# Kernel optimization log

Hardware: AMD Instinct MI355X
Metric: run time of the kernel (lower is better)

The kernel has to match this reference:

```python
import jax, jax.numpy as jnp
import numpy as np

N = 8192   # nodes
F = 128    # features
ORDER = 4  # polynomial taps


def setup_inputs() -> dict:
    key = jax.random.key(0)
    k1, k2, k3 = jax.random.split(key, 3)
    X = jax.random.normal(k1, (N, F), dtype=jnp.float32)
    # scale GSO so powers don't blow up (spectral-norm-ish normalization)
    S = jax.random.normal(k2, (N, N), dtype=jnp.float32) / jnp.sqrt(jnp.float32(N))
    coefficients = jax.random.uniform(k3, (ORDER,), dtype=jnp.float32)
    return {"X": X, "S": S, "coefficients": coefficients}


def reference(X, S, coefficients):
    # y = sum_{k=0}^{K-1} h_k * S^k X
    Z = X
    y = coefficients[0] * Z
    for k in range(1, ORDER):  # small fixed tap count; loop over taps, not data
        Z = S @ Z              # S^k X, [N, F]
        y = y + coefficients[k] * Z
    return y
```

## Files before the change

kernel.cpp:

```cpp
#include <hip/hip_runtime.h>
#include <hip/hip_bf16.h>
#include <stdint.h>


typedef __attribute__((ext_vector_type(8))) short     bf16x8;
typedef __attribute__((ext_vector_type(8))) uint16_t  u16x8;
typedef __attribute__((ext_vector_type(4))) float     f32x4;

#define NN 8192
#define NF 128
#define ZSTRIDE (8192 + 64)

#define WAITV(n) asm volatile("s_waitcnt vmcnt(" #n ")" ::: "memory")
#define WAITL0   asm volatile("s_waitcnt lgkmcnt(0)" ::: "memory")

__device__ inline uint16_t f2bf(float f) {
    uint32_t u = __builtin_bit_cast(uint32_t, f);
    u += 0x7fffu + ((u >> 16) & 1u);
    return (uint16_t)(u >> 16);
}

__device__ inline void gl2lds16(const void* g, uint8_t* l) {
    __builtin_amdgcn_global_load_lds(
        (const __attribute__((address_space(1))) uint32_t*)g,
        (__attribute__((address_space(3))) uint32_t*)l,
        16, 0, 0);
}

__device__ inline bf16x8 ld16(const uint8_t* p) {
    return __builtin_bit_cast(bf16x8, *(const u16x8*)p);
}

__global__ __launch_bounds__(256) void k_prep(const float* __restrict__ X,
                                              const float* __restrict__ coeff,
                                              float* __restrict__ y,
                                              uint16_t* __restrict__ ZT0) {
    __shared__ float tile[16][NF + 4];
    const int t  = threadIdx.x;
    const int r0 = blockIdx.x * 16;
    const float h0 = coeff[0];
#pragma unroll
    for (int i = 0; i < 2; ++i) {
        int o   = (i * 256 + t) * 4;
        int row = o >> 7, col = o & 127;
        f32x4 v = *(const f32x4*)(X + (size_t)(r0 + row) * NF + col);
        *(f32x4*)&tile[row][col] = v;
        *(f32x4*)(y + (size_t)(r0 + row) * NF + col) = v * h0;
    }
    __syncthreads();
    const int c = t >> 1, rh = t & 1;
    u16x8 pk;
#pragma unroll
    for (int e = 0; e < 8; ++e) pk[e] = f2bf(tile[rh * 8 + e][c]);
    *(u16x8*)(ZT0 + (size_t)c * ZSTRIDE + r0 + rh * 8) = pk;
}

template<int NT>
__device__ inline void gemm_core(const uint16_t* asrc, const uint16_t* bsrc,
                                 uint8_t* smem, int t, f32x4 (&acc)[4],
                                 int aoff, int bof) {
    auto stage = [&](int buf, int kt) {
        const int ko = kt * 64;
        uint8_t* b = smem + buf * 24576;
        gl2lds16(asrc + ko, b + t * 16);
        gl2lds16(bsrc + ko, b + 8192 + t * 16);
        gl2lds16(bsrc + (size_t)64 * ZSTRIDE + ko, b + 16384 + t * 16);
    };
    stage(0, 0);
    int cur = 0;
#pragma unroll 1
    for (int kt = 0; kt < NT; ++kt) {
        if (kt + 1 < NT) {
            stage(cur ^ 1, kt + 1);
            WAITV(3);
        } else {
            WAITV(0);
        }
        __builtin_amdgcn_s_barrier();
        __builtin_amdgcn_sched_barrier(0);
        const uint8_t* bb = smem + cur * 24576;
        bf16x8 a0 = ld16(bb + aoff);
        bf16x8 a1 = ld16(bb + (aoff ^ 64));
#pragma unroll
        for (int ct = 0; ct < 4; ++ct) {
            acc[ct] = __builtin_amdgcn_mfma_f32_16x16x32_bf16(
                a0, ld16(bb + bof + ct * 16 * 128), acc[ct], 0, 0, 0);
            acc[ct] = __builtin_amdgcn_mfma_f32_16x16x32_bf16(
                a1, ld16(bb + ((bof + ct * 16 * 128) ^ 64)), acc[ct], 0, 0, 0);
        }
        WAITL0;
        __builtin_amdgcn_sched_barrier(0);
        __builtin_amdgcn_s_barrier();
        cur ^= 1;
    }
}

template<int KS>
__global__ __launch_bounds__(512, 4) void k_gemm_bf(
    const uint16_t* __restrict__ S16, const uint16_t* __restrict__ ZTin,
    float* __restrict__ P)
{
    __shared__ __align__(16) uint8_t smem[2][24576];
    const int t = threadIdx.x, lane = t & 63;
    const int w = t >> 6, m = lane & 15, g = lane >> 4;
    const int rt = w & 3, ch = w >> 2;
    const int mt = blockIdx.x & 127, ks = blockIdx.x >> 7;
    const int r0 = mt * 64;
    const int kb = ks * (NN / KS);
    constexpr int NT = (NN / KS) / 64;

    const int srow = t >> 3, sc = t & 7;
    const int scs  = (sc ^ (srow & 7)) << 3;
    const uint16_t* asrc = S16  + (size_t)(r0 + srow) * NN + kb + scs;
    const uint16_t* bsrc = ZTin + (size_t)srow * ZSTRIDE   + kb + scs;

    const int sw   = m & 7;
    const int aoff = (rt * 16 + m) * 128 + ((g ^ sw) << 4);
    const int bof  = 8192 + (ch * 64 + m) * 128 + ((g ^ sw) << 4);

    f32x4 acc[4] = {};
    gemm_core<NT>(asrc, bsrc, &smem[0][0], t, acc, aoff, bof);

    float* pb = P + ((size_t)ks * NN + r0 + rt * 16 + 4 * g) * NF + ch * 64 + m;
#pragma unroll
    for (int ct = 0; ct < 4; ++ct)
#pragma unroll
        for (int i = 0; i < 4; ++i)
            pb[(size_t)i * NF + ct * 16] = acc[ct][i];
}

template<int KS>
__global__ __launch_bounds__(512, 4) void k_gemm_cv2(
    const float* __restrict__ Sf, const uint16_t* __restrict__ S16,
    const uint16_t* __restrict__ ZTin, float* __restrict__ P)
{
    __shared__ __align__(16) uint8_t smem[2][24576];
    const int t = threadIdx.x, lane = t & 63;
    const int w = t >> 6, m = lane & 15, g = lane >> 4;
    const int rt = w & 3, ch = w >> 2;
    const int mt = blockIdx.x & 127, ks = blockIdx.x >> 7;
    const int r0 = mt * 64;
    const int kb = ks * (NN / KS);
    constexpr int KSL = NN / KS;
    constexpr int NT  = KSL / 64;
    constexpr int C8  = KSL / 8;
    constexpr int ITERS = 64 * KSL / (512 * 8);

    uint16_t* S16w = (uint16_t*)S16;
#pragma unroll 4
    for (int it = 0; it < ITERS; ++it) {
        int id  = it * 512 + t;
        int row = id / C8, c8 = id % C8;
        size_t off = (size_t)(r0 + row) * NN + kb + c8 * 8;
        f32x4 a = *(const f32x4*)(Sf + off);
        f32x4 b = *(const f32x4*)(Sf + off + 4);
        u16x8 p;
#pragma unroll
        for (int j = 0; j < 4; ++j) { p[j] = f2bf(a[j]); p[j + 4] = f2bf(b[j]); }
        *(u16x8*)(S16w + off) = p;
    }
    WAITV(0);
    __syncthreads();

    const int srow = t >> 3, sc = t & 7;
    const int scs  = (sc ^ (srow & 7)) << 3;
    const uint16_t* asrc = S16  + (size_t)(r0 + srow) * NN + kb + scs;
    const uint16_t* bsrc = ZTin + (size_t)srow * ZSTRIDE   + kb + scs;

    const int sw   = m & 7;
    const int aoff = (rt * 16 + m) * 128 + ((g ^ sw) << 4);
    const int bof  = 8192 + (ch * 64 + m) * 128 + ((g ^ sw) << 4);

    f32x4 acc[4] = {};
    gemm_core<NT>(asrc, bsrc, &smem[0][0], t, acc, aoff, bof);

    float* pb = P + ((size_t)ks * NN + r0 + rt * 16 + 4 * g) * NF + ch * 64 + m;
#pragma unroll
    for (int ct = 0; ct < 4; ++ct)
#pragma unroll
        for (int i = 0; i < 4; ++i)
            pb[(size_t)i * NF + ct * 16] = acc[ct][i];
}

template<int KS, bool WRITE_ZT>
__global__ __launch_bounds__(256) void k_combine(const float* __restrict__ P,
                                                 float* __restrict__ y,
                                                 uint16_t* __restrict__ ZTout,
                                                 const float* __restrict__ coeff,
                                                 int pass) {
    __shared__ float tile[16][NF + 4];
    const int t = threadIdx.x, r0 = blockIdx.x * 16;
    const float hk = coeff[pass];
    const int row = t >> 4, col = (t & 15) * 8;
    const size_t off = (size_t)(r0 + row) * NF + col;
    f32x4 s0 = *(const f32x4*)(P + off);
    f32x4 s1 = *(const f32x4*)(P + off + 4);
#pragma unroll
    for (int k = 1; k < KS; ++k) {
        s0 += *(const f32x4*)(P + (size_t)k * NN * NF + off);
        s1 += *(const f32x4*)(P + (size_t)k * NN * NF + off + 4);
    }
    float* yp = y + off;
    f32x4 y0 = *(const f32x4*)yp, y1 = *(const f32x4*)(yp + 4);
    *(f32x4*)yp       = y0 + hk * s0;
    *(f32x4*)(yp + 4) = y1 + hk * s1;
    if (WRITE_ZT) {
        *(f32x4*)&tile[row][col]     = s0;
        *(f32x4*)&tile[row][col + 4] = s1;
        __syncthreads();
        const int c = t >> 1, rh = t & 1;
        u16x8 pk;
#pragma unroll
        for (int e = 0; e < 8; ++e) pk[e] = f2bf(tile[rh * 8 + e][c]);
        *(u16x8*)(ZTout + (size_t)c * ZSTRIDE + r0 + rh * 8) = pk;
    }
}

template<int KS>
static void run(const float* X, const float* S, const float* coeff, float* y,
                uint16_t* ZT0, uint16_t* ZT1, uint16_t* S16, float* P,
                hipStream_t stream) {
    k_prep<<<dim3(512), dim3(256), 0, stream>>>(X, coeff, y, ZT0);
    k_gemm_cv2<KS><<<dim3(128 * KS), dim3(512), 0, stream>>>(S, S16, ZT0, P);
    k_combine<KS, true ><<<dim3(512), dim3(256), 0, stream>>>(P, y, ZT1, coeff, 1);
    k_gemm_bf<KS><<<dim3(128 * KS), dim3(512), 0, stream>>>(S16, ZT1, P);
    k_combine<KS, true ><<<dim3(512), dim3(256), 0, stream>>>(P, y, ZT0, coeff, 2);
    k_gemm_bf<KS><<<dim3(128 * KS), dim3(512), 0, stream>>>(S16, ZT0, P);
    k_combine<KS, false><<<dim3(512), dim3(256), 0, stream>>>(P, y, nullptr, coeff, 3);
}

extern "C" void kernel_launch(void* const* d_in, const int* in_sizes, int n_in,
                              void* d_out, int out_size, void* d_ws, size_t ws_size,
                              hipStream_t stream) {
    const float* X     = (const float*)d_in[0];
    const float* S     = (const float*)d_in[1];
    const float* coeff = (const float*)d_in[2];
    float* y = (float*)d_out;

    uint8_t* ws = (uint8_t*)d_ws;
    const size_t zb     = ((size_t)NF * ZSTRIDE * sizeof(uint16_t) + 255) & ~(size_t)255;
    const size_t s16b   = (size_t)NN * NN * sizeof(uint16_t);
    const size_t base   = 2 * zb + s16b;
    const size_t pslice = (size_t)NN * NF * sizeof(float);
    uint16_t* ZT0 = (uint16_t*)ws;
    uint16_t* ZT1 = (uint16_t*)(ws + zb);
    uint16_t* S16 = (uint16_t*)(ws + 2 * zb);
    float*    P   = (float*)(ws + base);

    if (ws_size >= base + 4 * pslice)
        run<4>(X, S, coeff, y, ZT0, ZT1, S16, P, stream);
    else if (ws_size >= base + 2 * pslice)
        run<2>(X, S, coeff, y, ZT0, ZT1, S16, P, stream);
    else
        run<1>(X, S, coeff, y, ZT0, ZT1, S16, P, stream);
}
```

Before: 196.1 us.

## Fuse all stages into one persistent kernel with atomic grid barriers

Replaces the seven-launch sequence (prep, three GEMMs, three combines) with a single persistent kernel of 512 blocks that moves between stages using atomic-counter grid barriers. The barrier counters are zeroed with a memset before each launch. The goal is to remove per-launch overhead and the tail and idle time between dependent kernels. The risk is deadlock if all 512 blocks cannot be co-resident, plus spin-wait cost at each barrier. The fallback path now converts S to bf16 in a separate kernel instead of inside the first GEMM.

Result: slower. 673.9 us (+243.7%).

```diff
diff --git a/kernel.cpp b/kernel.cpp
--- a/kernel.cpp
+++ b/kernel.cpp
@@ -10,6 +10,7 @@
 #define NN 8192
 #define NF 128
 #define ZSTRIDE (8192 + 64)
+#define GRID 512
 
 #define WAITV(n) asm volatile("s_waitcnt vmcnt(" #n ")" ::: "memory")
 #define WAITL0   asm volatile("s_waitcnt lgkmcnt(0)" ::: "memory")
@@ -31,28 +32,20 @@
     return __builtin_bit_cast(bf16x8, *(const u16x8*)p);
 }
 
-__global__ __launch_bounds__(256) void k_prep(const float* __restrict__ X,
-                                              const float* __restrict__ coeff,
-                                              float* __restrict__ y,
-                                              uint16_t* __restrict__ ZT0) {
-    __shared__ float tile[16][NF + 4];
-    const int t  = threadIdx.x;
-    const int r0 = blockIdx.x * 16;
-    const float h0 = coeff[0];
-#pragma unroll
-    for (int i = 0; i < 2; ++i) {
-        int o   = (i * 256 + t) * 4;
-        int row = o >> 7, col = o & 127;
-        f32x4 v = *(const f32x4*)(X + (size_t)(r0 + row) * NF + col);
-        *(f32x4*)&tile[row][col] = v;
-        *(f32x4*)(y + (size_t)(r0 + row) * NF + col) = v * h0;
-    }
+__device__ inline void gridbar(uint32_t* ctr, int idx) {
     __syncthreads();
-    const int c = t >> 1, rh = t & 1;
-    u16x8 pk;
-#pragma unroll
-    for (int e = 0; e < 8; ++e) pk[e] = f2bf(tile[rh * 8 + e][c]);
-    *(u16x8*)(ZT0 + (size_t)c * ZSTRIDE + r0 + rh * 8) = pk;
+    if (threadIdx.x == 0) {
+        __threadfence();
+        __hip_atomic_fetch_add(ctr + idx, 1u, __ATOMIC_ACQ_REL,
+                               __HIP_MEMORY_SCOPE_AGENT);
+        uint32_t v;
+        do {
+            __builtin_amdgcn_s_sleep(2);
+            v = __hip_atomic_load(ctr + idx, __ATOMIC_ACQUIRE,
+                                  __HIP_MEMORY_SCOPE_AGENT);
+        } while (v < GRID);
+    }
+    __syncthreads();
 }
 
 template<int NT>
@@ -95,6 +88,149 @@
     }
 }
 
+
+__device__ void mega_gemm(const uint16_t* S16, const uint16_t* ZTin,
+                          float* P, uint8_t* smem, int mt, int ks, int t) {
+    const int lane = t & 63, w = t >> 6, m = lane & 15, g = lane >> 4;
+    const int rt = w & 3, ch = w >> 2;
+    const int r0 = mt * 64, kb = ks * 2048;
+    const int srow = t >> 3, sc = t & 7;
+    const int scs  = (sc ^ (srow & 7)) << 3;
+    const uint16_t* asrc = S16  + (size_t)(r0 + srow) * NN + kb + scs;
+    const uint16_t* bsrc = ZTin + (size_t)srow * ZSTRIDE   + kb + scs;
+    const int sw   = m & 7;
+    const int aoff = (rt * 16 + m) * 128 + ((g ^ sw) << 4);
+    const int bof  = 8192 + (ch * 64 + m) * 128 + ((g ^ sw) << 4);
+    f32x4 acc[4] = {};
+    gemm_core<32>(asrc, bsrc, smem, t, acc, aoff, bof);
+    float* pb = P + ((size_t)ks * NN + r0 + rt * 16 + 4 * g) * NF + ch * 64 + m;
+#pragma unroll
+    for (int ct = 0; ct < 4; ++ct)
+#pragma unroll
+        for (int i = 0; i < 4; ++i)
+            pb[(size_t)i * NF + ct * 16] = acc[ct][i];
+}
+
+__device__ void mega_combine(const float* P, float* y, uint16_t* ZTout,
+                             float hk, uint8_t* smem, int bx, int t) {
+    float* tile = (float*)smem;
+    const int r0 = bx * 16;
+    const int row = t >> 5, colc = t & 31;
+    const size_t off = (size_t)(r0 + row) * NF + colc * 4;
+    f32x4 s = *(const f32x4*)(P + off);
+#pragma unroll
+    for (int k = 1; k < 4; ++k)
+        s += *(const f32x4*)(P + (size_t)k * NN * NF + off);
+    f32x4 yv = *(const f32x4*)(y + off);
+    *(f32x4*)(y + off) = yv + hk * s;
+    if (ZTout) {
+        *(f32x4*)&tile[row * 132 + colc * 4] = s;
+        __syncthreads();
+        if (t < 256) {
+            const int c = t >> 1, rh = t & 1;
+            u16x8 pk;
+#pragma unroll
+            for (int e = 0; e < 8; ++e) pk[e] = f2bf(tile[(rh * 8 + e) * 132 + c]);
+            *(u16x8*)(ZTout + (size_t)c * ZSTRIDE + r0 + rh * 8) = pk;
+        }
+    }
+}
+
+__global__ __launch_bounds__(512, 4) void k_mega(
+    const float* __restrict__ S, const float* __restrict__ X,
+    const float* __restrict__ coeff, float* __restrict__ y,
+    uint16_t* ZT0, uint16_t* ZT1, uint16_t* S16, float* P, uint32_t* bar)
+{
+    __shared__ __align__(16) uint8_t smem[49152];
+    const int bx = blockIdx.x, t = threadIdx.x;
+    const int mt = bx & 127, ks = bx >> 7;
+    const int r0 = mt * 64, kb = ks * 2048;
+
+#pragma unroll 4
+    for (int it = 0; it < 32; ++it) {
+        int id  = it * 512 + t;
+        int row = id >> 8, c8 = id & 255;
+        size_t off = (size_t)(r0 + row) * NN + kb + c8 * 8;
+        f32x4 a = *(const f32x4*)(S + off);
+        f32x4 b = *(const f32x4*)(S + off + 4);
+        u16x8 p;
+#pragma unroll
+        for (int j = 0; j < 4; ++j) { p[j] = f2bf(a[j]); p[j + 4] = f2bf(b[j]); }
+        *(u16x8*)(S16 + off) = p;
+    }
+    {
+        float* tile = (float*)smem;
+        const int rp = bx * 16;
+        const float h0 = coeff[0];
+        const int row = t >> 5, colc = t & 31;
+        f32x4 v = *(const f32x4*)(X + (size_t)(rp + row) * NF + colc * 4);
+        *(f32x4*)&tile[row * 132 + colc * 4] = v;
+        *(f32x4*)(y + (size_t)(rp + row) * NF + colc * 4) = v * h0;
+        __syncthreads();
+        if (t < 256) {
+            const int c = t >> 1, rh = t & 1;
+            u16x8 pk;
+#pragma unroll
+            for (int e = 0; e < 8; ++e) pk[e] = f2bf(tile[(rh * 8 + e) * 132 + c]);
+            *(u16x8*)(ZT0 + (size_t)c * ZSTRIDE + rp + rh * 8) = pk;
+        }
+    }
+    gridbar(bar, 0);
+
+    mega_gemm(S16, ZT0, P, smem, mt, ks, t);
+    gridbar(bar, 1);
+    mega_combine(P, y, ZT1, coeff[1], smem, bx, t);
+    gridbar(bar, 2);
+
+    mega_gemm(S16, ZT1, P, smem, mt, ks, t);
+    gridbar(bar, 3);
+    mega_combine(P, y, ZT0, coeff[2], smem, bx, t);
+    gridbar(bar, 4);
+
+    mega_gemm(S16, ZT0, P, smem, mt, ks, t);
+    gridbar(bar, 5);
+    mega_combine(P, y, nullptr, coeff[3], smem, bx, t);
+}
+
+
+__global__ __launch_bounds__(256) void k_convert(const float* __restrict__ S,
+                                                 uint16_t* __restrict__ S16) {
+    const size_t n8 = (size_t)NN * NN / 8;
+    const size_t stride = (size_t)gridDim.x * 256;
+    for (size_t i = (size_t)blockIdx.x * 256 + threadIdx.x; i < n8; i += stride) {
+        f32x4 a = *(const f32x4*)(S + i * 8);
+        f32x4 b = *(const f32x4*)(S + i * 8 + 4);
+        u16x8 p;
+#pragma unroll
+        for (int j = 0; j < 4; ++j) { p[j] = f2bf(a[j]); p[j + 4] = f2bf(b[j]); }
+        *(u16x8*)(S16 + i * 8) = p;
+    }
+}
+
+__global__ __launch_bounds__(256) void k_prep(const float* __restrict__ X,
+                                              const float* __restrict__ coeff,
+                                              float* __restrict__ y,
+                                              uint16_t* __restrict__ ZT0) {
+    __shared__ float tile[16][NF + 4];
+    const int t  = threadIdx.x;
+    const int r0 = blockIdx.x * 16;
+    const float h0 = coeff[0];
+#pragma unroll
+    for (int i = 0; i < 2; ++i) {
+        int o   = (i * 256 + t) * 4;
+        int row = o >> 7, col = o & 127;
+        f32x4 v = *(const f32x4*)(X + (size_t)(r0 + row) * NF + col);
+        *(f32x4*)&tile[row][col] = v;
+        *(f32x4*)(y + (size_t)(r0 + row) * NF + col) = v * h0;
+    }
+    __syncthreads();
+    const int c = t >> 1, rh = t & 1;
+    u16x8 pk;
+#pragma unroll
+    for (int e = 0; e < 8; ++e) pk[e] = f2bf(tile[rh * 8 + e][c]);
+    *(u16x8*)(ZT0 + (size_t)c * ZSTRIDE + r0 + rh * 8) = pk;
+}
+
 template<int KS>
 __global__ __launch_bounds__(512, 4) void k_gemm_bf(
     const uint16_t* __restrict__ S16, const uint16_t* __restrict__ ZTin,
@@ -129,59 +265,6 @@
             pb[(size_t)i * NF + ct * 16] = acc[ct][i];
 }
 
-template<int KS>
-__global__ __launch_bounds__(512, 4) void k_gemm_cv2(
-    const float* __restrict__ Sf, const uint16_t* __restrict__ S16,
-    const uint16_t* __restrict__ ZTin, float* __restrict__ P)
-{
-    __shared__ __align__(16) uint8_t smem[2][24576];
-    const int t = threadIdx.x, lane = t & 63;
-    const int w = t >> 6, m = lane & 15, g = lane >> 4;
-    const int rt = w & 3, ch = w >> 2;
-    const int mt = blockIdx.x & 127, ks = blockIdx.x >> 7;
-    const int r0 = mt * 64;
-    const int kb = ks * (NN / KS);
-    constexpr int KSL = NN / KS;
-    constexpr int NT  = KSL / 64;
-    constexpr int C8  = KSL / 8;
-    constexpr int ITERS = 64 * KSL / (512 * 8);
-
-    uint16_t* S16w = (uint16_t*)S16;
-#pragma unroll 4
-    for (int it = 0; it < ITERS; ++it) {
-        int id  = it * 512 + t;
-        int row = id / C8, c8 = id % C8;
-        size_t off = (size_t)(r0 + row) * NN + kb + c8 * 8;
-        f32x4 a = *(const f32x4*)(Sf + off);
-        f32x4 b = *(const f32x4*)(Sf + off + 4);
-        u16x8 p;
-#pragma unroll
-        for (int j = 0; j < 4; ++j) { p[j] = f2bf(a[j]); p[j + 4] = f2bf(b[j]); }
-        *(u16x8*)(S16w + off) = p;
-    }
-    WAITV(0);
-    __syncthreads();
-
-    const int srow = t >> 3, sc = t & 7;
-    const int scs  = (sc ^ (srow & 7)) << 3;
-    const uint16_t* asrc = S16  + (size_t)(r0 + srow) * NN + kb + scs;
-    const uint16_t* bsrc = ZTin + (size_t)srow * ZSTRIDE   + kb + scs;
-
-    const int sw   = m & 7;
-    const int aoff = (rt * 16 + m) * 128 + ((g ^ sw) << 4);
-    const int bof  = 8192 + (ch * 64 + m) * 128 + ((g ^ sw) << 4);
-
-    f32x4 acc[4] = {};
-    gemm_core<NT>(asrc, bsrc, &smem[0][0], t, acc, aoff, bof);
-
-    float* pb = P + ((size_t)ks * NN + r0 + rt * 16 + 4 * g) * NF + ch * 64 + m;
-#pragma unroll
-    for (int ct = 0; ct < 4; ++ct)
-#pragma unroll
-        for (int i = 0; i < 4; ++i)
-            pb[(size_t)i * NF + ct * 16] = acc[ct][i];
-}
-
 template<int KS, bool WRITE_ZT>
 __global__ __launch_bounds__(256) void k_combine(const float* __restrict__ P,
                                                  float* __restrict__ y,
@@ -217,11 +300,12 @@
 }
 
 template<int KS>
-static void run(const float* X, const float* S, const float* coeff, float* y,
-                uint16_t* ZT0, uint16_t* ZT1, uint16_t* S16, float* P,
-                hipStream_t stream) {
+static void run_fallback(const float* X, const float* S, const float* coeff,
+                         float* y, uint16_t* ZT0, uint16_t* ZT1, uint16_t* S16,
+                         float* P, hipStream_t stream) {
     k_prep<<<dim3(512), dim3(256), 0, stream>>>(X, coeff, y, ZT0);
-    k_gemm_cv2<KS><<<dim3(128 * KS), dim3(512), 0, stream>>>(S, S16, ZT0, P);
+    k_convert<<<dim3(2048), dim3(256), 0, stream>>>(S, S16);
+    k_gemm_bf<KS><<<dim3(128 * KS), dim3(512), 0, stream>>>(S16, ZT0, P);
     k_combine<KS, true ><<<dim3(512), dim3(256), 0, stream>>>(P, y, ZT1, coeff, 1);
     k_gemm_bf<KS><<<dim3(128 * KS), dim3(512), 0, stream>>>(S16, ZT1, P);
     k_combine<KS, true ><<<dim3(512), dim3(256), 0, stream>>>(P, y, ZT0, coeff, 2);
@@ -246,11 +330,16 @@
     uint16_t* ZT1 = (uint16_t*)(ws + zb);
     uint16_t* S16 = (uint16_t*)(ws + 2 * zb);
     float*    P   = (float*)(ws + base);
-
-    if (ws_size >= base + 4 * pslice)
-        run<4>(X, S, coeff, y, ZT0, ZT1, S16, P, stream);
-    else if (ws_size >= base + 2 * pslice)
-        run<2>(X, S, coeff, y, ZT0, ZT1, S16, P, stream);
-    else
-        run<1>(X, S, coeff, y, ZT0, ZT1, S16, P, stream);
-}
+    const size_t bar_off = base + 4 * pslice;
+
+    if (ws_size >= bar_off + 256) {
+        uint32_t* bar = (uint32_t*)(ws + bar_off);
+        hipMemsetAsync(bar, 0, 64, stream);
+        k_mega<<<dim3(GRID), dim3(512), 0, stream>>>(S, X, coeff, y,
+                                                     ZT0, ZT1, S16, P, bar);
+    } else if (ws_size >= base + 2 * pslice) {
+        run_fallback<2>(X, S, coeff, y, ZT0, ZT1, S16, P, stream);
+    } else {
+        run_fallback<1>(X, S, coeff, y, ZT0, ZT1, S16, P, stream);
+    }
+}
```
